# Kernel tuning notes

Hardware: AMD Instinct MI355X
Metric: run time of the kernel (lower is better)

## Reference

```python
import jax, jax.numpy as jnp
import numpy as np

B, I, H, E, V, T = 512, 2560, 512, 300, 8000, 16
SOS = 2

def setup_inputs() -> dict:
    key = jax.random.key(0)
    ks = jax.random.split(key, 12)
    s = lambda k, shape: (jax.random.normal(k, shape, jnp.float32) * 0.05)
    emb = s(ks[2], (V, E)).at[0].set(0.0)  # padding_idx=0
    return dict(
        fused_features=jax.random.normal(ks[0], (B, I), jnp.float32),
        target_answers=jax.random.randint(ks[1], (B, T), 0, V),
        max_len=T,
        embedding=emb,
        W_in=s(ks[3], (H, I)), b_in=jnp.zeros((H,), jnp.float32),
        W_cell=s(ks[4], (H, I)), b_cell=jnp.zeros((H,), jnp.float32),
        W_ih0=s(ks[5], (4 * H, E + H)), W_hh0=s(ks[6], (4 * H, H)),
        b_ih0=jnp.zeros((4 * H,), jnp.float32), b_hh0=jnp.zeros((4 * H,), jnp.float32),
        W_ih1=s(ks[7], (4 * H, H)), W_hh1=s(ks[8], (4 * H, H)),
        b_ih1=jnp.zeros((4 * H,), jnp.float32), b_hh1=jnp.zeros((4 * H,), jnp.float32),
        W_out=s(ks[9], (V, H)), b_out=jnp.zeros((V,), jnp.float32),
    )

def _cell(gates, c):
    # PyTorch LSTM gate order: i, f, g, o
    i, f, g, o = jnp.split(gates, 4, axis=-1)
    c_new = jax.nn.sigmoid(f) * c + jax.nn.sigmoid(i) * jnp.tanh(g)
    h_new = jax.nn.sigmoid(o) * jnp.tanh(c_new)
    return h_new, c_new

def reference(fused_features, target_answers, max_len, embedding,
              W_in, b_in, W_cell, b_cell,
              W_ih0, W_hh0, b_ih0, b_hh0,
              W_ih1, W_hh1, b_ih1, b_hh1,
              W_out, b_out):
    context = fused_features @ W_in.T + b_in          # [B,H]
    cell0 = fused_features @ W_cell.T + b_cell        # [B,H]
    # teacher forcing (ratio=1.0, deterministic): inputs = [SOS, y_0..y_{T-2}]
    words = jnp.concatenate(
        [jnp.full((context.shape[0], 1), SOS, target_answers.dtype),
         target_answers[:, :-1]], axis=1)             # [B,T]
    emb = embedding[words]                            # [B,T,E]
    x = jnp.concatenate(
        [emb, jnp.broadcast_to(context[:, None, :], (emb.shape[0], emb.shape[1], context.shape[1]))],
        axis=-1)                                      # [B,T,E+H]
    # precompute input-side gates for layer 0 in one big GEMM
    xg0 = jnp.einsum('bti,gi->tbg', x, W_ih0) + b_ih0 + b_hh0  # [T,B,4H]

    def step(carry, xg):
        h0, c0, h1, c1 = carry
        h0, c0 = _cell(xg + h0 @ W_hh0.T, c0)
        h1, c1 = _cell(h0 @ W_ih1.T + b_ih1 + b_hh1 + h1 @ W_hh1.T, c1)
        return (h0, c0, h1, c1), h1

    init = (context, cell0, context, cell0)
    _, hs = jax.lax.scan(step, init, xg0)             # hs: [T,B,H]
    logits = jnp.einsum('tbh,vh->btv', hs, W_out) + b_out  # [B,T,V]
    return logits
```

## Files before the change

kernel.cpp:

```cpp
#include <hip/hip_runtime.h>
#include <cstdint>

#define B_   512
#define I_   2560
#define H_   512
#define E_   300
#define EW   320
#define V_   8000
#define VPAD 8064
#define T_   16
#define G4H  2048
#define SOS_ 2

typedef _Float16 f16;
typedef _Float16 f16x8 __attribute__((ext_vector_type(8)));
typedef _Float16 f16x4 __attribute__((ext_vector_type(4)));
typedef float    f32x4 __attribute__((ext_vector_type(4)));

__device__ __forceinline__ float sigmoidf_(float x) {
    return 1.0f / (1.0f + __expf(-x));
}

__device__ __forceinline__ void gload16(const void* g, void* l) {
    __builtin_amdgcn_global_load_lds(
        (const __attribute__((address_space(1))) void*)g,
        (__attribute__((address_space(3))) void*)l,
        16, 0, 0);
}

__global__ __launch_bounds__(256)
void gemm_mfma(const f16* __restrict__ A, int lda,
               const f16* __restrict__ Bw, int ldb,
               float* __restrict__ C, int ldc,
               int K, int Nvalid,
               const float* __restrict__ bias1,
               const float* __restrict__ bias2)
{
    __shared__ f16 As[128][32];
    __shared__ f16 Bs[128][32];

    const int tid  = threadIdx.x;
    const int w    = tid >> 6;
    const int lane = tid & 63;
    const int bm   = blockIdx.x * 128;
    const int bn   = blockIdx.y * 128;
    const int wr   = w >> 1;
    const int wc   = w & 1;

    const int srow = lane >> 2;
    const int skel = (lane & 3) * 8;

    const f16* Ag0 = A  + (size_t)(bm + w*32 +      srow) * lda + skel;
    const f16* Ag1 = A  + (size_t)(bm + w*32 + 16 + srow) * lda + skel;
    const f16* Bg0 = Bw + (size_t)(bn + w*32 +      srow) * ldb + skel;
    const f16* Bg1 = Bw + (size_t)(bn + w*32 + 16 + srow) * ldb + skel;
    f16* Al0 = &As[w*32     ][0];
    f16* Al1 = &As[w*32 + 16][0];
    f16* Bl0 = &Bs[w*32     ][0];
    f16* Bl1 = &Bs[w*32 + 16][0];

    const int frow = lane & 15;
    const int fk   = (lane >> 4) * 8;

    f32x4 acc[4][4] = {};

    for (int k0 = 0; k0 < K; k0 += 32) {
        gload16(Ag0 + k0, Al0);
        gload16(Ag1 + k0, Al1);
        gload16(Bg0 + k0, Bl0);
        gload16(Bg1 + k0, Bl1);
        __syncthreads();

        f16x8 af[4], bf[4];
        #pragma unroll
        for (int m = 0; m < 4; ++m)
            af[m] = *reinterpret_cast<const f16x8*>(&As[wr*64 + m*16 + frow][fk]);
        #pragma unroll
        for (int n = 0; n < 4; ++n)
            bf[n] = *reinterpret_cast<const f16x8*>(&Bs[wc*64 + n*16 + frow][fk]);

        #pragma unroll
        for (int m = 0; m < 4; ++m)
            #pragma unroll
            for (int n = 0; n < 4; ++n)
                acc[m][n] = __builtin_amdgcn_mfma_f32_16x16x32_f16(
                    af[m], bf[n], acc[m][n], 0, 0, 0);

        __syncthreads();
    }

    const int rowb = bm + wr*64 + (lane >> 4) * 4;
    #pragma unroll
    for (int n = 0; n < 4; ++n) {
        const int col = bn + wc*64 + n*16 + frow;
        if (col >= Nvalid) continue;
        float badd = 0.0f;
        if (bias1) badd += bias1[col];
        if (bias2) badd += bias2[col];
        #pragma unroll
        for (int m = 0; m < 4; ++m) {
            const int r0 = rowb + m*16;
            #pragma unroll
            for (int r = 0; r < 4; ++r)
                C[(size_t)(r0 + r) * ldc + col] = acc[m][n][r] + badd;
        }
    }
}

__device__ __forceinline__ void gemm_cell_body(
    const f16* __restrict__ Ap1, const f16* __restrict__ Ap2, int lda2,
    const f16* __restrict__ Wp, int K,
    const float* __restrict__ Cadd,
    const float* __restrict__ bih, const float* __restrict__ bhh,
    float* __restrict__ cst,
    f16* __restrict__ hout1,
    char* smem, int bm, int bn)
{
    const int tid  = threadIdx.x;
    const int w    = tid >> 6;
    const int lane = tid & 63;
    const int wr   = w >> 1, wc = w & 1;
    const int frow = lane & 15, hi = lane >> 4;
    const int sw   = (frow & 7) << 4;
    const int srow8 = lane >> 3;
    const int ksb  = ((((lane & 7) * 16) ^ (srow8 << 4)) >> 1);

    const int NT = K >> 6;
    f32x4 acc[2][4] = {};

    char* Abuf = smem;
    char* Wbuf = smem + 16384;

    auto stage = [&](int bsel, int kt) {
        const int k0 = kt << 6;
        #pragma unroll
        for (int j = 0; j < 2; ++j) {
            const int row = w*16 + j*8 + srow8;
            const f16* src;
            if (k0 < 512) src = Ap1 + (size_t)(bm + row) * 512  + k0 + ksb;
            else          src = Ap2 + (size_t)(bm + row) * lda2 + (k0 - 512) + ksb;
            gload16(src, Abuf + bsel*8192 + (w*2 + j)*1024 + lane*16);
        }
        #pragma unroll
        for (int j = 0; j < 4; ++j) {
            const int row = w*32 + j*8 + srow8;
            gload16(Wp + (size_t)(bn + row) * K + k0 + ksb,
                    Wbuf + bsel*16384 + (w*4 + j)*1024 + lane*16);
        }
    };

    stage(0, 0);
    stage(1, 1);

    int buf = 0;
    for (int kt = 0; kt < NT; ++kt) {
        if (kt < NT - 1) asm volatile("s_waitcnt vmcnt(6)" ::: "memory");
        else             asm volatile("s_waitcnt vmcnt(0)" ::: "memory");
        __builtin_amdgcn_sched_barrier(0);
        __builtin_amdgcn_s_barrier();
        __builtin_amdgcn_sched_barrier(0);

        const char* A_ = Abuf + buf*8192;
        const char* W_ = Wbuf + buf*16384;
        f16x8 af[2][2], bf[2][4];
        #pragma unroll
        for (int ks = 0; ks < 2; ++ks) {
            const int cb = (ks*64 + hi*16) ^ sw;
            #pragma unroll
            for (int m = 0; m < 2; ++m)
                af[ks][m] = *reinterpret_cast<const f16x8*>(A_ + (wr*32 + m*16 + frow)*128 + cb);
            #pragma unroll
            for (int n = 0; n < 4; ++n)
                bf[ks][n] = *reinterpret_cast<const f16x8*>(W_ + (wc*64 + n*16 + frow)*128 + cb);
        }
        __builtin_amdgcn_sched_barrier(0);
        asm volatile("s_waitcnt lgkmcnt(0)" ::: "memory");
        __builtin_amdgcn_sched_barrier(0);
        __builtin_amdgcn_s_barrier();
        __builtin_amdgcn_sched_barrier(0);

        if (kt + 2 < NT) stage(buf, kt + 2);

        #pragma unroll
        for (int ks = 0; ks < 2; ++ks)
            #pragma unroll
            for (int m = 0; m < 2; ++m)
                #pragma unroll
                for (int n = 0; n < 4; ++n)
                    acc[m][n] = __builtin_amdgcn_mfma_f32_16x16x32_f16(
                        af[ks][m], bf[ks][n], acc[m][n], 0, 0, 0);
        buf ^= 1;
    }

    float* gs = (float*)smem;
    #pragma unroll
    for (int m = 0; m < 2; ++m) {
        const int row = wr*32 + m*16 + hi*4;
        #pragma unroll
        for (int n = 0; n < 4; ++n) {
            const int col = wc*64 + n*16 + frow;
            #pragma unroll
            for (int r = 0; r < 4; ++r) {
                float v = acc[m][n][r];
                if (Cadd) v += Cadd[(size_t)(bm + row + r) * G4H + bn + col];
                gs[(row + r)*132 + col] = v;
            }
        }
    }
    __syncthreads();

    const int hp = tid & 31;
    const int hg = (bn >> 2) + hp;
    float bi0 = 0.f, bi1 = 0.f, bi2 = 0.f, bi3 = 0.f;
    if (bih) {
        bi0 = bih[hg]        + bhh[hg];
        bi1 = bih[512 + hg]  + bhh[512 + hg];
        bi2 = bih[1024 + hg] + bhh[1024 + hg];
        bi3 = bih[1536 + hg] + bhh[1536 + hg];
    }
    #pragma unroll
    for (int i = 0; i < 8; ++i) {
        const int r = (tid >> 5) * 8 + i;
        const int b = bm + r;
        const float gi = gs[r*132 +      hp] + bi0;
        const float gf = gs[r*132 + 32 + hp] + bi1;
        const float gc = gs[r*132 + 64 + hp] + bi2;
        const float go = gs[r*132 + 96 + hp] + bi3;
        const float c  = cst[(size_t)b * 512 + hg];
        const float cn = sigmoidf_(gf) * c + sigmoidf_(gi) * tanhf(gc);
        const float hn = sigmoidf_(go) * tanhf(cn);
        cst[(size_t)b * 512 + hg] = cn;
        hout1[(size_t)b * 512 + hg] = (f16)hn;
    }
}

__device__ __forceinline__ void gemm_out_body(
    const f16* __restrict__ A, const f16* __restrict__ Bw,
    float* __restrict__ C,
    const float* __restrict__ bias,
    int bm, int bn, char* smem, int tid)
{
    const int w    = tid >> 6;
    const int lane = tid & 63;
    const int wr   = w >> 1, wc = w & 1;
    const int srow = lane >> 2;
    const int skel = (lane & 3) * 8;
    const int frow = lane & 15;
    const int fk   = (lane >> 4) * 8;

    const f16* Ag0 = A  + (size_t)(bm + w*32 +      srow) * 512 + skel;
    const f16* Ag1 = A  + (size_t)(bm + w*32 + 16 + srow) * 512 + skel;
    const f16* Bg0 = Bw + (size_t)(bn + w*32 +      srow) * 512 + skel;
    const f16* Bg1 = Bw + (size_t)(bn + w*32 + 16 + srow) * 512 + skel;

    auto stage = [&](int bsel, int kt) {
        const int k0 = kt << 5;
        char* As_ = smem + bsel*8192;
        char* Bs_ = smem + 24576 + bsel*8192;
        gload16(Ag0 + k0, As_ + (w*32     )*64);
        gload16(Ag1 + k0, As_ + (w*32 + 16)*64);
        gload16(Bg0 + k0, Bs_ + (w*32     )*64);
        gload16(Bg1 + k0, Bs_ + (w*32 + 16)*64);
    };

    f32x4 acc[4][4] = {};

    stage(0, 0);
    stage(1, 1);
    stage(2, 2);

    int buf = 0;
    for (int kt = 0; kt < 16; ++kt) {
        const int rem = 15 - kt;
        if (rem >= 2)      asm volatile("s_waitcnt vmcnt(8)" ::: "memory");
        else if (rem == 1) asm volatile("s_waitcnt vmcnt(4)" ::: "memory");
        else               asm volatile("s_waitcnt vmcnt(0)" ::: "memory");
        __builtin_amdgcn_sched_barrier(0);
        __builtin_amdgcn_s_barrier();
        __builtin_amdgcn_sched_barrier(0);

        const char* As_ = smem + buf*8192;
        const char* Bs_ = smem + 24576 + buf*8192;
        f16x8 af[4], bf[4];
        #pragma unroll
        for (int m = 0; m < 4; ++m)
            af[m] = *reinterpret_cast<const f16x8*>(As_ + (wr*64 + m*16 + frow)*64 + fk*2);
        #pragma unroll
        for (int n = 0; n < 4; ++n)
            bf[n] = *reinterpret_cast<const f16x8*>(Bs_ + (wc*64 + n*16 + frow)*64 + fk*2);
        __builtin_amdgcn_sched_barrier(0);
        asm volatile("s_waitcnt lgkmcnt(0)" ::: "memory");
        __builtin_amdgcn_sched_barrier(0);
        __builtin_amdgcn_s_barrier();
        __builtin_amdgcn_sched_barrier(0);

        if (kt + 3 < 16) stage(buf, kt + 3);

        #pragma unroll
        for (int m = 0; m < 4; ++m)
            #pragma unroll
            for (int n = 0; n < 4; ++n)
                acc[m][n] = __builtin_amdgcn_mfma_f32_16x16x32_f16(
                    af[m], bf[n], acc[m][n], 0, 0, 0);
        buf = (buf == 2) ? 0 : buf + 1;
    }

    const int rowb = bm + wr*64 + (lane >> 4) * 4;
    #pragma unroll
    for (int n = 0; n < 4; ++n) {
        const int col = bn + wc*64 + n*16 + frow;
        if (col >= V_) continue;
        const float badd = bias[col];
        #pragma unroll
        for (int m = 0; m < 4; ++m) {
            const int r0 = rowb + m*16;
            #pragma unroll
            for (int r = 0; r < 4; ++r)
                C[(size_t)(r0 + r) * (T_ * V_) + col] = acc[m][n][r] + badd;
        }
    }
}

__global__ __launch_bounds__(256)
void phase_kernel(const f16* __restrict__ h0in,
                  const f16* __restrict__ embt,
                  f16* __restrict__ h0out,
                  const f16* __restrict__ h1in,
                  f16* __restrict__ h1out,
                  const f16* __restrict__ W0p, const f16* __restrict__ W1p,
                  const f16* __restrict__ WoutP,
                  const float* __restrict__ ctxg,
                  const float* __restrict__ bih1, const float* __restrict__ bhh1,
                  const float* __restrict__ b_out,
                  float* __restrict__ c0, float* __restrict__ c1,
                  float* __restrict__ out, int tout,
                  int active0, int active1, int activeO)
{
    __shared__ char smem[49152];
    const int bx = blockIdx.x;

    if (bx < 128) {
        if (!active0) return;
        const int xcd = bx & 7, idx = bx >> 3;
        const int bn = (xcd*2 + (idx & 1)) * 128;
        const int bm = (idx >> 1) * 64;
        gemm_cell_body(h0in, embt, EW, W0p, 832,
                       ctxg, nullptr, nullptr, c0, h0out, smem, bm, bn);
    } else if (bx < 256) {
        if (!active1) return;
        const int lb = bx - 128;
        const int xcd = lb & 7, idx = lb >> 3;
        const int bn = (xcd*2 + (idx & 1)) * 128;
        const int bm = (idx >> 1) * 64;
        gemm_cell_body(h0in, h1in, 512, W1p, 1024,
                       nullptr, bih1, bhh1, c1, h1out, smem, bm, bn);
    } else {
        if (!activeO) return;
        const int o = bx - 256;
        const int xcd = o & 7, j = o >> 3;
        const int bnt = xcd*8 + (j >> 2);
        if (bnt >= 63) return;
        const int bm = (j & 3) * 128;
        gemm_out_body(h1in, WoutP, out + (size_t)tout * V_, b_out,
                      bm, bnt * 128, smem, threadIdx.x);
    }
}

__global__ __launch_bounds__(256)
void conv_f16_k(const float* __restrict__ src, f16* __restrict__ dst)
{
    const int i = blockIdx.x * 256 + threadIdx.x;
    const float4 v = reinterpret_cast<const float4*>(src)[i];
    f16x4 h = { (f16)v.x, (f16)v.y, (f16)v.z, (f16)v.w };
    *reinterpret_cast<f16x4*>(dst + (size_t)i * 4) = h;
}

__global__ __launch_bounds__(256)
void pack_wincell(const float* __restrict__ Win, const float* __restrict__ Wcell,
                  f16* __restrict__ dst)
{
    const int i = blockIdx.x * 256 + threadIdx.x;
    const int r = i / 640, c4 = (i % 640) * 4;
    const float* src = (r < 512) ? Win + (size_t)r * I_ + c4
                                 : Wcell + (size_t)(r - 512) * I_ + c4;
    const float4 v = *reinterpret_cast<const float4*>(src);
    f16x4 h = { (f16)v.x, (f16)v.y, (f16)v.z, (f16)v.w };
    *reinterpret_cast<f16x4*>(dst + (size_t)i * 4) = h;
}

__global__ __launch_bounds__(256)
void pack_w0p(const float* __restrict__ Whh0, const float* __restrict__ Wih0,
              f16* __restrict__ W0)
{
    const int idx = blockIdx.x * 256 + threadIdx.x;
    const int rp = idx / 832, k = idx % 832;
    const int g = (rp >> 5) & 3, h = (rp >> 7) * 32 + (rp & 31);
    const int srow = g * 512 + h;
    float v;
    if (k < 512)      v = Whh0[(size_t)srow * 512 + k];
    else if (k < 812) v = Wih0[(size_t)srow * 812 + (k - 512)];
    else              v = 0.0f;
    W0[idx] = (f16)v;
}

__global__ __launch_bounds__(256)
void pack_w1p(const float* __restrict__ Wih1, const float* __restrict__ Whh1,
              f16* __restrict__ W1)
{
    const int idx = blockIdx.x * 256 + threadIdx.x;
    const int rp = idx >> 10, k = idx & 1023;
    const int g = (rp >> 5) & 3, h = (rp >> 7) * 32 + (rp & 31);
    const int srow = g * 512 + h;
    const float v = (k < 512) ? Wih1[(size_t)srow * 512 + k]
                              : Whh1[(size_t)srow * 512 + (k - 512)];
    W1[idx] = (f16)v;
}

__global__ __launch_bounds__(256)
void pack_wctxp(const float* __restrict__ Wih0, f16* __restrict__ Wc)
{
    const int idx = blockIdx.x * 256 + threadIdx.x;
    const int rp = idx >> 9, k = idx & 511;
    const int g = (rp >> 5) & 3, h = (rp >> 7) * 32 + (rp & 31);
    Wc[idx] = (f16)Wih0[(size_t)(g * 512 + h) * 812 + 300 + k];
}

__global__ __launch_bounds__(256)
void pack_b0(const float* __restrict__ bih0, const float* __restrict__ bhh0,
             float* __restrict__ b01p)
{
    const int idx = blockIdx.x * 256 + threadIdx.x;
    const int g = (idx >> 5) & 3, h = (idx >> 7) * 32 + (idx & 31);
    b01p[idx] = bih0[g * 512 + h] + bhh0[g * 512 + h];
}

__global__ __launch_bounds__(256)
void pack_wout(const float* __restrict__ Wout, f16* __restrict__ Wo)
{
    const int i = blockIdx.x * 256 + threadIdx.x;
    const int r = i >> 7, c4 = (i & 127) * 4;
    f16x4 h = { (f16)0.f, (f16)0.f, (f16)0.f, (f16)0.f };
    if (r < V_) {
        const float4 v = *reinterpret_cast<const float4*>(Wout + (size_t)r * H_ + c4);
        h = f16x4{ (f16)v.x, (f16)v.y, (f16)v.z, (f16)v.w };
    }
    *reinterpret_cast<f16x4*>(Wo + (size_t)i * 4) = h;
}

__global__ __launch_bounds__(256)
void pack_emb_all(const float* __restrict__ emb, const int* __restrict__ target,
                  f16* __restrict__ embAll)
{
    const int idx = blockIdx.x * 256 + threadIdx.x;
    const int t = idx / (B_ * EW);
    const int rem = idx % (B_ * EW);
    const int b = rem / EW, e = rem % EW;
    const int wd = (t == 0) ? SOS_ : target[b * T_ + (t - 1)];
    const float v = (e < E_) ? emb[(size_t)wd * E_ + e] : 0.0f;
    embAll[idx] = (f16)v;
}

__global__ __launch_bounds__(256)
void init_state(const float* __restrict__ ctxcc,
                const float* __restrict__ b_in, const float* __restrict__ b_cell,
                f16* __restrict__ ctx16, f16* __restrict__ h0, f16* __restrict__ h1,
                float* __restrict__ c0, float* __restrict__ c1)
{
    const int idx = blockIdx.x * 256 + threadIdx.x;
    const int b = idx >> 9, h = idx & 511;
    const float cv = ctxcc[(size_t)b * 1024 + h] + b_in[h];
    const float cc = ctxcc[(size_t)b * 1024 + 512 + h] + b_cell[h];
    const f16 ch = (f16)cv;
    ctx16[idx] = ch;
    h0[idx] = ch;
    h1[idx] = ch;
    c0[idx] = cc;
    c1[idx] = cc;
}

extern "C" void kernel_launch(void* const* d_in, const int* in_sizes, int n_in,
                              void* d_out, int out_size, void* d_ws, size_t ws_size,
                              hipStream_t stream)
{
    const float* fused  = (const float*)d_in[0];
    const int*   target = (const int*)d_in[1];
    const float* emb    = (const float*)d_in[3];
    const float* W_in   = (const float*)d_in[4];
    const float* b_in   = (const float*)d_in[5];
    const float* W_cell = (const float*)d_in[6];
    const float* b_cell = (const float*)d_in[7];
    const float* W_ih0  = (const float*)d_in[8];
    const float* W_hh0  = (const float*)d_in[9];
    const float* b_ih0  = (const float*)d_in[10];
    const float* b_hh0  = (const float*)d_in[11];
    const float* W_ih1  = (const float*)d_in[12];
    const float* W_hh1  = (const float*)d_in[13];
    const float* b_ih1  = (const float*)d_in[14];
    const float* b_hh1  = (const float*)d_in[15];
    const float* W_out  = (const float*)d_in[16];
    const float* b_out  = (const float*)d_in[17];
    float* out = (float*)d_out;

    char* p = (char*)d_ws;
    auto carve = [&](size_t bytes) {
        char* r = p;
        p += (bytes + 255) & ~(size_t)255;
        return r;
    };
    float* ctxcc  = (float*)carve((size_t)B_ * 1024 * 4);
    float* ctxg   = (float*)carve((size_t)B_ * G4H * 4);
    float* b01p   = (float*)carve((size_t)G4H * 4);
    float* c0     = (float*)carve((size_t)B_ * H_ * 4);
    float* c1     = (float*)carve((size_t)B_ * H_ * 4);
    f16* fused16  = (f16*)carve((size_t)B_ * I_ * 2);
    f16* WinCell  = (f16*)carve((size_t)1024 * I_ * 2);
    f16* W0p      = (f16*)carve((size_t)G4H * 832 * 2);
    f16* W1p      = (f16*)carve((size_t)G4H * 1024 * 2);
    f16* Wctxp    = (f16*)carve((size_t)G4H * H_ * 2);
    f16* Wout16   = (f16*)carve((size_t)VPAD * H_ * 2);
    f16* ctx16    = (f16*)carve((size_t)B_ * H_ * 2);
    f16* h0a      = (f16*)carve((size_t)B_ * H_ * 2);
    f16* h0b      = (f16*)carve((size_t)B_ * H_ * 2);
    f16* h1a      = (f16*)carve((size_t)B_ * H_ * 2);
    f16* h1b      = (f16*)carve((size_t)B_ * H_ * 2);
    f16* embAll   = (f16*)carve((size_t)T_ * B_ * EW * 2);

    conv_f16_k  <<<(B_ * I_) / 1024, 256, 0, stream>>>(fused, fused16);
    pack_wincell<<<(1024 * I_) / 1024, 256, 0, stream>>>(W_in, W_cell, WinCell);
    pack_w0p    <<<(G4H * 832) / 256, 256, 0, stream>>>(W_hh0, W_ih0, W0p);
    pack_w1p    <<<(G4H * 1024) / 256, 256, 0, stream>>>(W_ih1, W_hh1, W1p);
    pack_wctxp  <<<(G4H * H_) / 256, 256, 0, stream>>>(W_ih0, Wctxp);
    pack_b0     <<<G4H / 256, 256, 0, stream>>>(b_ih0, b_hh0, b01p);
    pack_wout   <<<(VPAD * H_) / 1024, 256, 0, stream>>>(W_out, Wout16);
    pack_emb_all<<<(T_ * B_ * EW) / 256, 256, 0, stream>>>(emb, target, embAll);

    gemm_mfma<<<dim3(B_/128, 1024/128), 256, 0, stream>>>(
        fused16, I_, WinCell, I_, ctxcc, 1024, I_, 1024, nullptr, nullptr);

    init_state<<<(B_ * H_) / 256, 256, 0, stream>>>(
        ctxcc, b_in, b_cell, ctx16, h0b, h1b, c0, c1);

    gemm_mfma<<<dim3(B_/128, G4H/128), 256, 0, stream>>>(
        ctx16, H_, Wctxp, H_, ctxg, G4H, H_, G4H, b01p, nullptr);

    f16* h0buf[2] = { h0a, h0b };
    f16* h1buf[2] = { h1a, h1b };
    for (int phase = 0; phase <= T_ + 1; ++phase) {
        const int a0 = (phase < T_) ? 1 : 0;
        const int a1 = (phase >= 1 && phase <= T_) ? 1 : 0;
        const int aO = (phase >= 2) ? 1 : 0;
        const int te = (phase < T_) ? phase : (T_ - 1);
        const int tO = aO ? (phase - 2) : 0;
        phase_kernel<<<dim3(512), 256, 0, stream>>>(
            h0buf[(phase + 1) & 1],
            embAll + (size_t)te * B_ * EW,
            h0buf[phase & 1],
            h1buf[phase & 1],
            h1buf[(phase + 1) & 1],
            W0p, W1p, Wout16, ctxg, b_ih1, b_hh1, b_out,
            c0, c1, out, tO, a0, a1, aO);
    }
}
```

Baseline: 483.8 us.

## Merge pack kernels, fuse init into ctx GEMM, retile output GEMM with swizzle

Folds the eight separate pack/convert kernels into one launch and fuses the init_state epilogue into the context/cell GEMM, which drops the ctxcc intermediate and cuts launch count. The output-projection GEMM inside the phase kernel moves from K=32 triple buffering to K=64 double buffering with an XOR-swizzled LDS layout to reduce bank conflicts. Its logits stores become nontemporal. Shared memory in the phase kernel grows to 64KB, which may lower occupancy.

```diff
diff --git a/kernel.cpp b/kernel.cpp
--- a/kernel.cpp
+++ b/kernel.cpp
@@ -33,8 +33,7 @@
                const f16* __restrict__ Bw, int ldb,
                float* __restrict__ C, int ldc,
                int K, int Nvalid,
-               const float* __restrict__ bias1,
-               const float* __restrict__ bias2)
+               const float* __restrict__ bias1)
 {
     __shared__ f16 As[128][32];
     __shared__ f16 Bs[128][32];
@@ -94,15 +93,100 @@
     for (int n = 0; n < 4; ++n) {
         const int col = bn + wc*64 + n*16 + frow;
         if (col >= Nvalid) continue;
-        float badd = 0.0f;
-        if (bias1) badd += bias1[col];
-        if (bias2) badd += bias2[col];
+        const float badd = bias1 ? bias1[col] : 0.0f;
         #pragma unroll
         for (int m = 0; m < 4; ++m) {
             const int r0 = rowb + m*16;
             #pragma unroll
             for (int r = 0; r < 4; ++r)
                 C[(size_t)(r0 + r) * ldc + col] = acc[m][n][r] + badd;
+        }
+    }
+}
+
+__global__ __launch_bounds__(256)
+void gemm_ctx_init(const f16* __restrict__ A,
+                   const f16* __restrict__ Bw,
+                   const float* __restrict__ b_in,
+                   const float* __restrict__ b_cell,
+                   f16* __restrict__ ctx16,
+                   f16* __restrict__ h0, f16* __restrict__ h1,
+                   float* __restrict__ c0, float* __restrict__ c1)
+{
+    __shared__ f16 As[128][32];
+    __shared__ f16 Bs[128][32];
+
+    const int tid  = threadIdx.x;
+    const int w    = tid >> 6;
+    const int lane = tid & 63;
+    const int bm   = blockIdx.x * 128;
+    const int bn   = blockIdx.y * 128;
+    const int wr   = w >> 1;
+    const int wc   = w & 1;
+
+    const int srow = lane >> 2;
+    const int skel = (lane & 3) * 8;
+
+    const f16* Ag0 = A  + (size_t)(bm + w*32 +      srow) * I_ + skel;
+    const f16* Ag1 = A  + (size_t)(bm + w*32 + 16 + srow) * I_ + skel;
+    const f16* Bg0 = Bw + (size_t)(bn + w*32 +      srow) * I_ + skel;
+    const f16* Bg1 = Bw + (size_t)(bn + w*32 + 16 + srow) * I_ + skel;
+    f16* Al0 = &As[w*32     ][0];
+    f16* Al1 = &As[w*32 + 16][0];
+    f16* Bl0 = &Bs[w*32     ][0];
+    f16* Bl1 = &Bs[w*32 + 16][0];
+
+    const int frow = lane & 15;
+    const int fk   = (lane >> 4) * 8;
+
+    f32x4 acc[4][4] = {};
+
+    for (int k0 = 0; k0 < I_; k0 += 32) {
+        gload16(Ag0 + k0, Al0);
+        gload16(Ag1 + k0, Al1);
+        gload16(Bg0 + k0, Bl0);
+        gload16(Bg1 + k0, Bl1);
+        __syncthreads();
+
+        f16x8 af[4], bf[4];
+        #pragma unroll
+        for (int m = 0; m < 4; ++m)
+            af[m] = *reinterpret_cast<const f16x8*>(&As[wr*64 + m*16 + frow][fk]);
+        #pragma unroll
+        for (int n = 0; n < 4; ++n)
+            bf[n] = *reinterpret_cast<const f16x8*>(&Bs[wc*64 + n*16 + frow][fk]);
+
+        #pragma unroll
+        for (int m = 0; m < 4; ++m)
+            #pragma unroll
+            for (int n = 0; n < 4; ++n)
+                acc[m][n] = __builtin_amdgcn_mfma_f32_16x16x32_f16(
+                    af[m], bf[n], acc[m][n], 0, 0, 0);
+
+        __syncthreads();
+    }
+
+    const int rowb = bm + wr*64 + (lane >> 4) * 4;
+    #pragma unroll
+    for (int n = 0; n < 4; ++n) {
+        const int col = bn + wc*64 + n*16 + frow;
+        #pragma unroll
+        for (int m = 0; m < 4; ++m) {
+            const int r0 = rowb + m*16;
+            #pragma unroll
+            for (int r = 0; r < 4; ++r) {
+                const int row = r0 + r;
+                if (col < 512) {
+                    const f16 ch = (f16)(acc[m][n][r] + b_in[col]);
+                    ctx16[(size_t)row * 512 + col] = ch;
+                    h0[(size_t)row * 512 + col] = ch;
+                    h1[(size_t)row * 512 + col] = ch;
+                } else {
+                    const float cc = acc[m][n][r] + b_cell[col - 512];
+                    c0[(size_t)row * 512 + col - 512] = cc;
+                    c1[(size_t)row * 512 + col - 512] = cc;
+                }
+            }
         }
     }
 }
@@ -243,66 +327,68 @@
     const int w    = tid >> 6;
     const int lane = tid & 63;
     const int wr   = w >> 1, wc = w & 1;
-    const int srow = lane >> 2;
-    const int skel = (lane & 3) * 8;
-    const int frow = lane & 15;
-    const int fk   = (lane >> 4) * 8;
-
-    const f16* Ag0 = A  + (size_t)(bm + w*32 +      srow) * 512 + skel;
-    const f16* Ag1 = A  + (size_t)(bm + w*32 + 16 + srow) * 512 + skel;
-    const f16* Bg0 = Bw + (size_t)(bn + w*32 +      srow) * 512 + skel;
-    const f16* Bg1 = Bw + (size_t)(bn + w*32 + 16 + srow) * 512 + skel;
+    const int frow = lane & 15, hi = lane >> 4;
+    const int sw   = (frow & 7) << 4;
+    const int srow8 = lane >> 3;
+    const int ksb  = ((((lane & 7) * 16) ^ (srow8 << 4)) >> 1);
+
+    char* Abuf = smem;
+    char* Wbuf = smem + 32768;
+    f32x4 acc[4][4] = {};
 
     auto stage = [&](int bsel, int kt) {
-        const int k0 = kt << 5;
-        char* As_ = smem + bsel*8192;
-        char* Bs_ = smem + 24576 + bsel*8192;
-        gload16(Ag0 + k0, As_ + (w*32     )*64);
-        gload16(Ag1 + k0, As_ + (w*32 + 16)*64);
-        gload16(Bg0 + k0, Bs_ + (w*32     )*64);
-        gload16(Bg1 + k0, Bs_ + (w*32 + 16)*64);
+        const int k0 = kt << 6;
+        #pragma unroll
+        for (int j = 0; j < 4; ++j) {
+            const int row = w*32 + j*8 + srow8;
+            gload16(A  + (size_t)(bm + row) * 512 + k0 + ksb,
+                    Abuf + bsel*16384 + (w*4 + j)*1024 + lane*16);
+            gload16(Bw + (size_t)(bn + row) * 512 + k0 + ksb,
+                    Wbuf + bsel*16384 + (w*4 + j)*1024 + lane*16);
+        }
     };
-
-    f32x4 acc[4][4] = {};
 
     stage(0, 0);
     stage(1, 1);
-    stage(2, 2);
 
     int buf = 0;
-    for (int kt = 0; kt < 16; ++kt) {
-        const int rem = 15 - kt;
-        if (rem >= 2)      asm volatile("s_waitcnt vmcnt(8)" ::: "memory");
-        else if (rem == 1) asm volatile("s_waitcnt vmcnt(4)" ::: "memory");
-        else               asm volatile("s_waitcnt vmcnt(0)" ::: "memory");
+    for (int kt = 0; kt < 8; ++kt) {
+        if (kt < 7) asm volatile("s_waitcnt vmcnt(8)" ::: "memory");
+        else        asm volatile("s_waitcnt vmcnt(0)" ::: "memory");
         __builtin_amdgcn_sched_barrier(0);
         __builtin_amdgcn_s_barrier();
         __builtin_amdgcn_sched_barrier(0);
 
-        const char* As_ = smem + buf*8192;
-        const char* Bs_ = smem + 24576 + buf*8192;
-        f16x8 af[4], bf[4];
-        #pragma unroll
-        for (int m = 0; m < 4; ++m)
-            af[m] = *reinterpret_cast<const f16x8*>(As_ + (wr*64 + m*16 + frow)*64 + fk*2);
-        #pragma unroll
-        for (int n = 0; n < 4; ++n)
-            bf[n] = *reinterpret_cast<const f16x8*>(Bs_ + (wc*64 + n*16 + frow)*64 + fk*2);
+        const char* A_ = Abuf + buf*16384;
+        const char* W_ = Wbuf + buf*16384;
+        f16x8 af[2][4], bf[2][4];
+        #pragma unroll
+        for (int ks = 0; ks < 2; ++ks) {
+            const int cb = (ks*64 + hi*16) ^ sw;
+            #pragma unroll
+            for (int m = 0; m < 4; ++m)
+                af[ks][m] = *reinterpret_cast<const f16x8*>(A_ + (wr*64 + m*16 + frow)*128 + cb);
+            #pragma unroll
+            for (int n = 0; n < 4; ++n)
+                bf[ks][n] = *reinterpret_cast<const f16x8*>(W_ + (wc*64 + n*16 + frow)*128 + cb);
+        }
         __builtin_amdgcn_sched_barrier(0);
         asm volatile("s_waitcnt lgkmcnt(0)" ::: "memory");
         __builtin_amdgcn_sched_barrier(0);
         __builtin_amdgcn_s_barrier();
         __builtin_amdgcn_sched_barrier(0);
 
-        if (kt + 3 < 16) stage(buf, kt + 3);
-
-        #pragma unroll
-        for (int m = 0; m < 4; ++m)
-            #pragma unroll
-            for (int n = 0; n < 4; ++n)
-                acc[m][n] = __builtin_amdgcn_mfma_f32_16x16x32_f16(
-                    af[m], bf[n], acc[m][n], 0, 0, 0);
-        buf = (buf == 2) ? 0 : buf + 1;
+        if (kt + 2 < 8) stage(buf, kt + 2);
+
+        #pragma unroll
+        for (int ks = 0; ks < 2; ++ks)
+            #pragma unroll
+            for (int m = 0; m < 4; ++m)
+                #pragma unroll
+                for (int n = 0; n < 4; ++n)
+                    acc[m][n] = __builtin_amdgcn_mfma_f32_16x16x32_f16(
+                        af[ks][m], bf[ks][n], acc[m][n], 0, 0, 0);
+        buf ^= 1;
     }
 
     const int rowb = bm + wr*64 + (lane >> 4) * 4;
@@ -316,7 +402,9 @@
             const int r0 = rowb + m*16;
             #pragma unroll
             for (int r = 0; r < 4; ++r)
-                C[(size_t)(r0 + r) * (T_ * V_) + col] = acc[m][n][r] + badd;
+                __builtin_nontemporal_store(
+                    acc[m][n][r] + badd,
+                    &C[(size_t)(r0 + r) * (T_ * V_) + col]);
         }
     }
 }
@@ -336,7 +424,7 @@
                   float* __restrict__ out, int tout,
                   int active0, int active1, int activeO)
 {
-    __shared__ char smem[49152];
+    __shared__ char smem[65536];
     const int bx = blockIdx.x;
 
     if (bx < 128) {
@@ -366,116 +454,111 @@
     }
 }
 
+#define NB_F16   1280
+#define NB_WIC   2560
+#define NB_W0    6656
+#define NB_W1    8192
+#define NB_WCTX  4096
+#define NB_B0    8
+#define NB_WOUT  4032
+#define NB_EMB   10240
+#define NB_TOTAL (NB_F16+NB_WIC+NB_W0+NB_W1+NB_WCTX+NB_B0+NB_WOUT+NB_EMB)
+
 __global__ __launch_bounds__(256)
-void conv_f16_k(const float* __restrict__ src, f16* __restrict__ dst)
+void pack_all(const float* __restrict__ fused,
+              const float* __restrict__ Win, const float* __restrict__ Wcell,
+              const float* __restrict__ Whh0, const float* __restrict__ Wih0,
+              const float* __restrict__ Wih1, const float* __restrict__ Whh1,
+              const float* __restrict__ bih0, const float* __restrict__ bhh0,
+              const float* __restrict__ Wout,
+              const float* __restrict__ emb, const int* __restrict__ target,
+              f16* __restrict__ fused16, f16* __restrict__ WinCell,
+              f16* __restrict__ W0, f16* __restrict__ W1,
+              f16* __restrict__ Wc, float* __restrict__ b01p,
+              f16* __restrict__ Wo, f16* __restrict__ embAll)
 {
-    const int i = blockIdx.x * 256 + threadIdx.x;
-    const float4 v = reinterpret_cast<const float4*>(src)[i];
-    f16x4 h = { (f16)v.x, (f16)v.y, (f16)v.z, (f16)v.w };
-    *reinterpret_cast<f16x4*>(dst + (size_t)i * 4) = h;
-}
-
-__global__ __launch_bounds__(256)
-void pack_wincell(const float* __restrict__ Win, const float* __restrict__ Wcell,
-                  f16* __restrict__ dst)
-{
-    const int i = blockIdx.x * 256 + threadIdx.x;
-    const int r = i / 640, c4 = (i % 640) * 4;
-    const float* src = (r < 512) ? Win + (size_t)r * I_ + c4
-                                 : Wcell + (size_t)(r - 512) * I_ + c4;
-    const float4 v = *reinterpret_cast<const float4*>(src);
-    f16x4 h = { (f16)v.x, (f16)v.y, (f16)v.z, (f16)v.w };
-    *reinterpret_cast<f16x4*>(dst + (size_t)i * 4) = h;
-}
-
-__global__ __launch_bounds__(256)
-void pack_w0p(const float* __restrict__ Whh0, const float* __restrict__ Wih0,
-              f16* __restrict__ W0)
-{
-    const int idx = blockIdx.x * 256 + threadIdx.x;
-    const int rp = idx / 832, k = idx % 832;
-    const int g = (rp >> 5) & 3, h = (rp >> 7) * 32 + (rp & 31);
-    const int srow = g * 512 + h;
-    float v;
-    if (k < 512)      v = Whh0[(size_t)srow * 512 + k];
-    else if (k < 812) v = Wih0[(size_t)srow * 812 + (k - 512)];
-    else              v = 0.0f;
-    W0[idx] = (f16)v;
-}
-
-__global__ __launch_bounds__(256)
-void pack_w1p(const float* __restrict__ Wih1, const float* __restrict__ Whh1,
-              f16* __restrict__ W1)
-{
-    const int idx = blockIdx.x * 256 + threadIdx.x;
-    const int rp = idx >> 10, k = idx & 1023;
-    const int g = (rp >> 5) & 3, h = (rp >> 7) * 32 + (rp & 31);
-    const int srow = g * 512 + h;
-    const float v = (k < 512) ? Wih1[(size_t)srow * 512 + k]
-                              : Whh1[(size_t)srow * 512 + (k - 512)];
-    W1[idx] = (f16)v;
-}
-
-__global__ __launch_bounds__(256)
-void pack_wctxp(const float* __restrict__ Wih0, f16* __restrict__ Wc)
-{
-    const int idx = blockIdx.x * 256 + threadIdx.x;
-    const int rp = idx >> 9, k = idx & 511;
-    const int g = (rp >> 5) & 3, h = (rp >> 7) * 32 + (rp & 31);
-    Wc[idx] = (f16)Wih0[(size_t)(g * 512 + h) * 812 + 300 + k];
-}
-
-__global__ __launch_bounds__(256)
-void pack_b0(const float* __restrict__ bih0, const float* __restrict__ bhh0,
-             float* __restrict__ b01p)
-{
-    const int idx = blockIdx.x * 256 + threadIdx.x;
-    const int g = (idx >> 5) & 3, h = (idx >> 7) * 32 + (idx & 31);
-    b01p[idx] = bih0[g * 512 + h] + bhh0[g * 512 + h];
-}
-
-__global__ __launch_bounds__(256)
-void pack_wout(const float* __restrict__ Wout, f16* __restrict__ Wo)
-{
-    const int i = blockIdx.x * 256 + threadIdx.x;
-    const int r = i >> 7, c4 = (i & 127) * 4;
-    f16x4 h = { (f16)0.f, (f16)0.f, (f16)0.f, (f16)0.f };
-    if (r < V_) {
-        const float4 v = *reinterpret_cast<const float4*>(Wout + (size_t)r * H_ + c4);
-        h = f16x4{ (f16)v.x, (f16)v.y, (f16)v.z, (f16)v.w };
-    }
-    *reinterpret_cast<f16x4*>(Wo + (size_t)i * 4) = h;
-}
-
-__global__ __launch_bounds__(256)
-void pack_emb_all(const float* __restrict__ emb, const int* __restrict__ target,
-                  f16* __restrict__ embAll)
-{
-    const int idx = blockIdx.x * 256 + threadIdx.x;
-    const int t = idx / (B_ * EW);
-    const int rem = idx % (B_ * EW);
-    const int b = rem / EW, e = rem % EW;
-    const int wd = (t == 0) ? SOS_ : target[b * T_ + (t - 1)];
-    const float v = (e < E_) ? emb[(size_t)wd * E_ + e] : 0.0f;
-    embAll[idx] = (f16)v;
-}
-
-__global__ __launch_bounds__(256)
-void init_state(const float* __restrict__ ctxcc,
-                const float* __restrict__ b_in, const float* __restrict__ b_cell,
-                f16* __restrict__ ctx16, f16* __restrict__ h0, f16* __restrict__ h1,
-                float* __restrict__ c0, float* __restrict__ c1)
-{
-    const int idx = blockIdx.x * 256 + threadIdx.x;
-    const int b = idx >> 9, h = idx & 511;
-    const float cv = ctxcc[(size_t)b * 1024 + h] + b_in[h];
-    const float cc = ctxcc[(size_t)b * 1024 + 512 + h] + b_cell[h];
-    const f16 ch = (f16)cv;
-    ctx16[idx] = ch;
-    h0[idx] = ch;
-    h1[idx] = ch;
-    c0[idx] = cc;
-    c1[idx] = cc;
+    int bx = blockIdx.x;
+    const int tid = threadIdx.x;
+
+    if (bx < NB_F16) {
+        const int i = bx * 256 + tid;
+        const float4 v = reinterpret_cast<const float4*>(fused)[i];
+        f16x4 h = { (f16)v.x, (f16)v.y, (f16)v.z, (f16)v.w };
+        *reinterpret_cast<f16x4*>(fused16 + (size_t)i * 4) = h;
+        return;
+    }
+    bx -= NB_F16;
+    if (bx < NB_WIC) {
+        const int i = bx * 256 + tid;
+        const int r = i / 640, c4 = (i % 640) * 4;
+        const float* src = (r < 512) ? Win + (size_t)r * I_ + c4
+                                     : Wcell + (size_t)(r - 512) * I_ + c4;
+        const float4 v = *reinterpret_cast<const float4*>(src);
+        f16x4 h = { (f16)v.x, (f16)v.y, (f16)v.z, (f16)v.w };
+        *reinterpret_cast<f16x4*>(WinCell + (size_t)i * 4) = h;
+        return;
+    }
+    bx -= NB_WIC;
+    if (bx < NB_W0) {
+        const int idx = bx * 256 + tid;
+        const int rp = idx / 832, k = idx % 832;
+        const int g = (rp >> 5) & 3, h = (rp >> 7) * 32 + (rp & 31);
+        const int srow = g * 512 + h;
+        float v;
+        if (k < 512)      v = Whh0[(size_t)srow * 512 + k];
+        else if (k < 812) v = Wih0[(size_t)srow * 812 + (k - 512)];
+        else              v = 0.0f;
+        W0[idx] = (f16)v;
+        return;
+    }
+    bx -= NB_W0;
+    if (bx < NB_W1) {
+        const int idx = bx * 256 + tid;
+        const int rp = idx >> 10, k = idx & 1023;
+        const int g = (rp >> 5) & 3, h = (rp >> 7) * 32 + (rp & 31);
+        const int srow = g * 512 + h;
+        const float v = (k < 512) ? Wih1[(size_t)srow * 512 + k]
+                                  : Whh1[(size_t)srow * 512 + (k - 512)];
+        W1[idx] = (f16)v;
+        return;
+    }
+    bx -= NB_W1;
+    if (bx < NB_WCTX) {
+        const int idx = bx * 256 + tid;
+        const int rp = idx >> 9, k = idx & 511;
+        const int g = (rp >> 5) & 3, h = (rp >> 7) * 32 + (rp & 31);
+        Wc[idx] = (f16)Wih0[(size_t)(g * 512 + h) * 812 + 300 + k];
+        return;
+    }
+    bx -= NB_WCTX;
+    if (bx < NB_B0) {
+        const int idx = bx * 256 + tid;
+        const int g = (idx >> 5) & 3, h = (idx >> 7) * 32 + (idx & 31);
+        b01p[idx] = bih0[g * 512 + h] + bhh0[g * 512 + h];
+        return;
+    }
+    bx -= NB_B0;
+    if (bx < NB_WOUT) {
+        const int i = bx * 256 + tid;
+        const int r = i >> 7, c4 = (i & 127) * 4;
+        f16x4 h = { (f16)0.f, (f16)0.f, (f16)0.f, (f16)0.f };
+        if (r < V_) {
+            const float4 v = *reinterpret_cast<const float4*>(Wout + (size_t)r * H_ + c4);
+            h = f16x4{ (f16)v.x, (f16)v.y, (f16)v.z, (f16)v.w };
+        }
+        *reinterpret_cast<f16x4*>(Wo + (size_t)i * 4) = h;
+        return;
+    }
+    bx -= NB_WOUT;
+    {
+        const int idx = bx * 256 + tid;
+        const int t = idx / (B_ * EW);
+        const int rem = idx % (B_ * EW);
+        const int b = rem / EW, e = rem % EW;
+        const int wd = (t == 0) ? SOS_ : target[b * T_ + (t - 1)];
+        const float v = (e < E_) ? emb[(size_t)wd * E_ + e] : 0.0f;
+        embAll[idx] = (f16)v;
+    }
 }
 
 extern "C" void kernel_launch(void* const* d_in, const int* in_sizes, int n_in,
@@ -507,7 +590,6 @@
         p += (bytes + 255) & ~(size_t)255;
         return r;
     };
-    float* ctxcc  = (float*)carve((size_t)B_ * 1024 * 4);
     float* ctxg   = (float*)carve((size_t)B_ * G4H * 4);
     float* b01p   = (float*)carve((size_t)G4H * 4);
     float* c0     = (float*)carve((size_t)B_ * H_ * 4);
@@ -525,23 +607,16 @@
     f16* h1b      = (f16*)carve((size_t)B_ * H_ * 2);
     f16* embAll   = (f16*)carve((size_t)T_ * B_ * EW * 2);
 
-    conv_f16_k  <<<(B_ * I_) / 1024, 256, 0, stream>>>(fused, fused16);
-    pack_wincell<<<(1024 * I_) / 1024, 256, 0, stream>>>(W_in, W_cell, WinCell);
-    pack_w0p    <<<(G4H * 832) / 256, 256, 0, stream>>>(W_hh0, W_ih0, W0p);
-    pack_w1p    <<<(G4H * 1024) / 256, 256, 0, stream>>>(W_ih1, W_hh1, W1p);
-    pack_wctxp  <<<(G4H * H_) / 256, 256, 0, stream>>>(W_ih0, Wctxp);
-    pack_b0     <<<G4H / 256, 256, 0, stream>>>(b_ih0, b_hh0, b01p);
-    pack_wout   <<<(VPAD * H_) / 1024, 256, 0, stream>>>(W_out, Wout16);
-    pack_emb_all<<<(T_ * B_ * EW) / 256, 256, 0, stream>>>(emb, target, embAll);
-
-    gemm_mfma<<<dim3(B_/128, 1024/128), 256, 0, stream>>>(
-        fused16, I_, WinCell, I_, ctxcc, 1024, I_, 1024, nullptr, nullptr);
-
-    init_state<<<(B_ * H_) / 256, 256, 0, stream>>>(
-        ctxcc, b_in, b_cell, ctx16, h0b, h1b, c0, c1);
+    pack_all<<<dim3(NB_TOTAL), 256, 0, stream>>>(
+        fused, W_in, W_cell, W_hh0, W_ih0, W_ih1, W_hh1,
+        b_ih0, b_hh0, W_out, emb, target,
+        fused16, WinCell, W0p, W1p, Wctxp, b01p, Wout16, embAll);
+
+    gemm_ctx_init<<<dim3(B_/128, 1024/128), 256, 0, stream>>>(
+        fused16, WinCell, b_in, b_cell, ctx16, h0b, h1b, c0, c1);
 
     gemm_mfma<<<dim3(B_/128, G4H/128), 256, 0, stream>>>(
-        ctx16, H_, Wctxp, H_, ctxg, G4H, H_, G4H, b01p, nullptr);
+        ctx16, H_, Wctxp, H_, ctxg, G4H, H_, G4H, b01p);
 
     f16* h0buf[2] = { h0a, h0b };
     f16* h1buf[2] = { h1a, h1b };
```

Result: faster. 447.2 us (-7.6%).
